# Kernel optimization log

Measured on AMD Instinct MI355X. Metric: run time of the kernel, lower is better.

Reference implementation:

```python
import jax, jax.numpy as jnp
import numpy as np

B, S, C = 16, 4096, 512


def setup_inputs() -> dict:
    key = jax.random.key(0)
    k1, k2, k3 = jax.random.split(key, 3)
    tag_logits_batch = jax.random.normal(k1, (B, S, C), dtype=jnp.float32)
    # probabilistic targets: normalize uniform draws so rows sum to 1
    t = jax.random.uniform(k2, (B, S, C), dtype=jnp.float32)
    target = t / jnp.sum(t, axis=-1, keepdims=True)
    mask = jax.random.randint(k3, (B, S), 0, 2, dtype=jnp.int32)
    return {"tag_logits_batch": tag_logits_batch, "target": target, "mask": mask}


def reference(tag_logits_batch, target, mask):
    # Soft-label cross-entropy per token: -sum_y target_y * log_softmax(logits)_y
    logp = jax.nn.log_softmax(tag_logits_batch, axis=-1)        # [B,S,C]
    tok_loss = -jnp.sum(target * logp, axis=-1)                  # [B,S]
    m = (mask == 1).astype(tok_loss.dtype)                       # [B,S]
    cnt = jnp.sum(m, axis=1)                                     # [B]
    # mean over active tokens per batch element (reduction='mean')
    per_batch = jnp.sum(tok_loss * m, axis=1) / jnp.maximum(cnt, 1.0)
    # torch code skips batch rows with no active tokens, then means over the rest
    has = (cnt > 0).astype(per_batch.dtype)                      # [B]
    return jnp.sum(per_batch * has) / jnp.maximum(jnp.sum(has), 1.0)
```

## Files before the change

### kernel.cpp

```cpp
#include <hip/hip_runtime.h>
#include <hip/hip_bf16.h>

#define BB 16
#define SS 4096
#define CC 512
#define NTOK (BB * SS)
#define LOSS_BLOCKS 2048
#define WAVES_TOTAL (LOSS_BLOCKS * 4)
#define WPB (WAVES_TOTAL / BB)


__global__ __launch_bounds__(256) void compact_kernel(
    const int* __restrict__ mask,
    int*       __restrict__ idxbuf,
    int*       __restrict__ cursors,
    float*     __restrict__ acc) {
    const int t     = blockIdx.x * 256 + threadIdx.x;
    const int batch = blockIdx.x / 16;
    const int lane  = threadIdx.x & 63;
    const int wave  = threadIdx.x >> 6;

    const bool active = (mask[t] == 1);
    unsigned long long ball = __ballot(active);
    const int prefix = __popcll(ball & ((1ull << lane) - 1ull));
    const int wcount = __popcll(ball);

    __shared__ int wbase[4];
    __shared__ int blockbase;
    if (lane == 0) wbase[wave] = wcount;
    __syncthreads();
    if (threadIdx.x == 0) {
        int total = wbase[0] + wbase[1] + wbase[2] + wbase[3];
        blockbase = atomicAdd(&cursors[batch], total);
        atomicAdd(&acc[2 * batch + 1], (float)total);
        int s = 0;
        for (int i = 0; i < 4; ++i) { int c = wbase[i]; wbase[i] = s; s += c; }
    }
    __syncthreads();
    if (active)
        idxbuf[batch * SS + blockbase + wbase[wave] + prefix] = t;
}

__global__ __launch_bounds__(256, 8) void loss_kernel(
    const float* __restrict__ logits,
    const float* __restrict__ target,
    const int*   __restrict__ idxbuf,
    const int*   __restrict__ cursors,
    float*       __restrict__ acc) {
    const int wave  = threadIdx.x >> 6;
    const int lane  = threadIdx.x & 63;
    const int wid   = blockIdx.x * 4 + wave;
    const int batch = wid & (BB - 1);
    const int w2    = wid >> 4;
    const int cnt   = cursors[batch];
    const int* list = idxbuf + batch * SS;

    float dotAcc = 0.0f;
    float logAcc = 0.0f;

    int k = w2;
    bool have = (k < cnt);
    float4 x0, x1, t0, t1;
    if (have) {
        const int tok = list[k];
        const float4* xp = (const float4*)(logits + (size_t)tok * CC);
        const float4* tp = (const float4*)(target + (size_t)tok * CC);
        x0 = xp[lane]; x1 = xp[lane + 64];
        t0 = tp[lane]; t1 = tp[lane + 64];
    }
    while (have) {
        const int kn = k + WPB;
        const bool haveN = (kn < cnt);
        float4 nx0, nx1, nt0, nt1;
        if (haveN) {
            const int tokN = list[kn];
            const float4* xp = (const float4*)(logits + (size_t)tokN * CC);
            const float4* tp = (const float4*)(target + (size_t)tokN * CC);
            nx0 = xp[lane]; nx1 = xp[lane + 64];
            nt0 = tp[lane]; nt1 = tp[lane + 64];
        }
        float se = __expf(x0.x) + __expf(x0.y) + __expf(x0.z) + __expf(x0.w)
                 + __expf(x1.x) + __expf(x1.y) + __expf(x1.z) + __expf(x1.w);
        dotAcc += t0.x * x0.x + t0.y * x0.y + t0.z * x0.z + t0.w * x0.w
                + t1.x * x1.x + t1.y * x1.y + t1.z * x1.z + t1.w * x1.w;
        #pragma unroll
        for (int off = 32; off >= 1; off >>= 1)
            se += __shfl_xor(se, off, 64);
        logAcc += __logf(se);
        x0 = nx0; x1 = nx1; t0 = nt0; t1 = nt1;
        k = kn; have = haveN;
    }

    #pragma unroll
    for (int off = 32; off >= 1; off >>= 1)
        dotAcc += __shfl_xor(dotAcc, off, 64);

    if (lane == 0) {
        float contrib = logAcc - dotAcc;
        if (contrib != 0.0f) atomicAdd(&acc[2 * batch], contrib);
    }
}

__global__ __launch_bounds__(64) void finalize_kernel(
    const float* __restrict__ acc,
    float*       __restrict__ out) {
    const int lane = threadIdx.x;
    float pb = 0.0f, has = 0.0f;
    if (lane < BB) {
        float s = acc[2 * lane];
        float c = acc[2 * lane + 1];
        if (c > 0.0f) { pb = s / c; has = 1.0f; }
    }
    #pragma unroll
    for (int off = 32; off >= 1; off >>= 1) {
        pb  += __shfl_xor(pb, off, 64);
        has += __shfl_xor(has, off, 64);
    }
    if (lane == 0) out[0] = pb / fmaxf(has, 1.0f);
}

extern "C" void kernel_launch(void* const* d_in, const int* in_sizes, int n_in,
                              void* d_out, int out_size, void* d_ws, size_t ws_size,
                              hipStream_t stream) {
    const float* logits = (const float*)d_in[0];
    const float* target = (const float*)d_in[1];
    const int*   mask   = (const int*)d_in[2];
    float* out     = (float*)d_out;
    float* acc     = (float*)d_ws;
    int*   cursors = (int*)((char*)d_ws + 128);
    int*   idxbuf  = (int*)((char*)d_ws + 256);

    hipMemsetAsync(d_ws, 0, 192, stream);
    compact_kernel<<<NTOK / 256, 256, 0, stream>>>(mask, idxbuf, cursors, acc);
    loss_kernel<<<LOSS_BLOCKS, 256, 0, stream>>>(logits, target, idxbuf, cursors, acc);
    finalize_kernel<<<1, 64, 0, stream>>>(acc, out);
}
```

Measured before the change: 292.6 us.

## Replace float atomics with per-block partials and a deterministic finalize reduction

The loss kernel now gives each batch a contiguous range of 128 blocks. It writes one partial sum per block instead of doing a float atomicAdd per wave. The compact kernel drops its count atomic, and finalize reads the cursor counts directly and reduces the 2048 partials with a 1024-thread block. This removes atomic contention and shrinks the memset, at the cost of a block-level __syncthreads and a heavier finalize launch; block-to-batch assignment also changes how work interleaves across batches.

```diff
diff --git a/kernel.cpp b/kernel.cpp
--- a/kernel.cpp
+++ b/kernel.cpp
@@ -6,15 +6,14 @@
 #define CC 512
 #define NTOK (BB * SS)
 #define LOSS_BLOCKS 2048
-#define WAVES_TOTAL (LOSS_BLOCKS * 4)
-#define WPB (WAVES_TOTAL / BB)
+#define BLOCKS_PER_BATCH (LOSS_BLOCKS / BB)
+#define WPB (BLOCKS_PER_BATCH * 4)
 
 
 __global__ __launch_bounds__(256) void compact_kernel(
     const int* __restrict__ mask,
     int*       __restrict__ idxbuf,
-    int*       __restrict__ cursors,
-    float*     __restrict__ acc) {
+    int*       __restrict__ cursors) {
     const int t     = blockIdx.x * 256 + threadIdx.x;
     const int batch = blockIdx.x / 16;
     const int lane  = threadIdx.x & 63;
@@ -32,7 +31,6 @@
     if (threadIdx.x == 0) {
         int total = wbase[0] + wbase[1] + wbase[2] + wbase[3];
         blockbase = atomicAdd(&cursors[batch], total);
-        atomicAdd(&acc[2 * batch + 1], (float)total);
         int s = 0;
         for (int i = 0; i < 4; ++i) { int c = wbase[i]; wbase[i] = s; s += c; }
     }
@@ -46,19 +44,18 @@
     const float* __restrict__ target,
     const int*   __restrict__ idxbuf,
     const int*   __restrict__ cursors,
-    float*       __restrict__ acc) {
+    float*       __restrict__ partial) {
     const int wave  = threadIdx.x >> 6;
     const int lane  = threadIdx.x & 63;
-    const int wid   = blockIdx.x * 4 + wave;
-    const int batch = wid & (BB - 1);
-    const int w2    = wid >> 4;
+    const int batch = blockIdx.x >> 7;
+    const int wib   = (blockIdx.x & (BLOCKS_PER_BATCH - 1)) * 4 + wave;
     const int cnt   = cursors[batch];
     const int* list = idxbuf + batch * SS;
 
     float dotAcc = 0.0f;
     float logAcc = 0.0f;
 
-    int k = w2;
+    int k = wib;
     bool have = (k < cnt);
     float4 x0, x1, t0, t1;
     if (have) {
@@ -95,28 +92,38 @@
     for (int off = 32; off >= 1; off >>= 1)
         dotAcc += __shfl_xor(dotAcc, off, 64);
 
-    if (lane == 0) {
-        float contrib = logAcc - dotAcc;
-        if (contrib != 0.0f) atomicAdd(&acc[2 * batch], contrib);
-    }
+    __shared__ float ls[4];
+    if (lane == 0) ls[wave] = logAcc - dotAcc;
+    __syncthreads();
+    if (threadIdx.x == 0)
+        partial[blockIdx.x] = ls[0] + ls[1] + ls[2] + ls[3];
 }
 
-__global__ __launch_bounds__(64) void finalize_kernel(
-    const float* __restrict__ acc,
+__global__ __launch_bounds__(1024) void finalize_kernel(
+    const float* __restrict__ partial,
+    const int*   __restrict__ cursors,
     float*       __restrict__ out) {
-    const int lane = threadIdx.x;
-    float pb = 0.0f, has = 0.0f;
-    if (lane < BB) {
-        float s = acc[2 * lane];
-        float c = acc[2 * lane + 1];
-        if (c > 0.0f) { pb = s / c; has = 1.0f; }
+    const int wave = threadIdx.x >> 6;
+    const int lane = threadIdx.x & 63;
+
+    float s = partial[wave * BLOCKS_PER_BATCH + lane]
+            + partial[wave * BLOCKS_PER_BATCH + 64 + lane];
+    #pragma unroll
+    for (int off = 32; off >= 1; off >>= 1)
+        s += __shfl_xor(s, off, 64);
+
+    __shared__ float pb[BB], has[BB];
+    if (lane == 0) {
+        float c = (float)cursors[wave];
+        pb[wave]  = (c > 0.0f) ? s / c : 0.0f;
+        has[wave] = (c > 0.0f) ? 1.0f : 0.0f;
     }
-    #pragma unroll
-    for (int off = 32; off >= 1; off >>= 1) {
-        pb  += __shfl_xor(pb, off, 64);
-        has += __shfl_xor(has, off, 64);
+    __syncthreads();
+    if (threadIdx.x == 0) {
+        float acc = 0.0f, nb = 0.0f;
+        for (int b = 0; b < BB; ++b) { acc += pb[b]; nb += has[b]; }
+        out[0] = acc / fmaxf(nb, 1.0f);
     }
-    if (lane == 0) out[0] = pb / fmaxf(has, 1.0f);
 }
 
 extern "C" void kernel_launch(void* const* d_in, const int* in_sizes, int n_in,
@@ -126,12 +133,12 @@
     const float* target = (const float*)d_in[1];
     const int*   mask   = (const int*)d_in[2];
     float* out     = (float*)d_out;
-    float* acc     = (float*)d_ws;
-    int*   cursors = (int*)((char*)d_ws + 128);
-    int*   idxbuf  = (int*)((char*)d_ws + 256);
+    int*   cursors = (int*)d_ws;
+    int*   idxbuf  = (int*)((char*)d_ws + 128);
+    float* partial = (float*)((char*)d_ws + 128 + NTOK * 4);
 
-    hipMemsetAsync(d_ws, 0, 192, stream);
-    compact_kernel<<<NTOK / 256, 256, 0, stream>>>(mask, idxbuf, cursors, acc);
-    loss_kernel<<<LOSS_BLOCKS, 256, 0, stream>>>(logits, target, idxbuf, cursors, acc);
-    finalize_kernel<<<1, 64, 0, stream>>>(acc, out);
+    hipMemsetAsync(cursors, 0, 64, stream);
+    compact_kernel<<<NTOK / 256, 256, 0, stream>>>(mask, idxbuf, cursors);
+    loss_kernel<<<LOSS_BLOCKS, 256, 0, stream>>>(logits, target, idxbuf, cursors, partial);
+    finalize_kernel<<<1, 1024, 0, stream>>>(partial, cursors, out);
 }
```

Result: faster. 255.8 us (-12.6%).
